# Kernel optimization log

Hardware: AMD Instinct MI355X
Metric: run time of the kernel (lower is better)

The kernel has to match this reference:

```python
import jax, jax.numpy as jnp
import numpy as np

N, MAX_DEG, F_IN, F_OUT = 20000, 32, 128, 128
TRIM_RATIO = 0.45
N_NEIGH_THRESHOLD = 3


def setup_inputs() -> dict:
    key = jax.random.key(0)
    k_h, k_nbr, k_deg, k_w, k_b = jax.random.split(key, 5)
    h = jax.random.normal(k_h, (N, F_IN), dtype=jnp.float32)
    nbr = jax.random.randint(k_nbr, (N, MAX_DEG), 0, N, dtype=jnp.int32)
    # in-degree in [1, MAX_DEG] so every node has at least one neighbor
    deg = jax.random.randint(k_deg, (N,), 1, MAX_DEG + 1, dtype=jnp.int32)
    # GCN symmetric normalizer deg^-0.5, per node, shape [N, 1]
    norm = (deg.astype(jnp.float32) ** -0.5)[:, None]
    stdv = 1.0 / np.sqrt(F_OUT)
    weight = jax.random.uniform(k_w, (F_IN, F_OUT), jnp.float32, -stdv, stdv)
    bias = jax.random.uniform(k_b, (F_OUT,), jnp.float32, -stdv, stdv)
    return {"h": h, "norm": norm, "weight": weight, "bias": bias,
            "nbr": nbr, "deg": deg}


def reference(h, norm, weight, bias, nbr, deg):
    # h: [N,F] node features (dropout=0 so input_ft == dropped_h == h)
    # nbr: [N,D] padded src indices; deg: [N] valid neighbor counts; norm: [N,1]
    D = nbr.shape[1]
    slot = jnp.arange(D, dtype=deg.dtype)[None, :]            # [1,D]
    valid = slot < deg[:, None]                                # [N,D]

    h_nbr = h[nbr]                                             # [N,D,F] = mailbox input_ft
    msg = h_nbr * norm[nbr]                                    # [N,D,F] = mailbox m (src h * src norm)

    # padded slots -> +inf so they sort past all valid entries (ranks >= deg)
    big = jnp.asarray(jnp.finfo(h.dtype).max, h.dtype)
    ift = jnp.where(valid[..., None], h_nbr, big)
    sidx = jnp.argsort(ift, axis=1)                            # per-feature sort over neighbors
    gathered = jnp.take_along_axis(msg, sidx, axis=1)          # [N,D,F]

    n = deg                                                    # per-node n_neigh
    b_raw = n // 2 - (1 - n % 2)
    b_cap = jnp.floor(n.astype(jnp.float32) * TRIM_RATIO).astype(n.dtype)
    b = jnp.maximum(jnp.minimum(b_raw, b_cap), 1)              # trim count per node

    # keep sorted ranks in [b, n-b)
    sel = (slot >= b[:, None]) & (slot < (n - b)[:, None])     # [N,D]
    trimmed_sum = jnp.sum(gathered * sel[..., None].astype(h.dtype), axis=1)  # [N,F]

    self0 = h * norm                                           # dst h * dst norm (mailbox 'self'[:,0])
    alpha = (2 * b).astype(h.dtype)[:, None]
    accum_med = (trimmed_sum + self0 * alpha) * norm           # trim_compensate=True branch
    accum_small = (n.astype(h.dtype)[:, None] * self0) * norm  # n_neigh <= threshold branch
    accum = jnp.where((n <= N_NEIGH_THRESHOLD)[:, None], accum_small, accum_med)

    # NodeApplyModule_V2: linear + bias + relu
    out = jax.nn.relu(accum @ weight + bias)
    return out
```

## Files before the change

### kernel.cpp

```cpp
#include <hip/hip_runtime.h>
#include <cfloat>
#include <cmath>

#define N_NODES 20000
#define MAXD 32
#define F 128


template <int SZ, int NV>
__device__ __forceinline__ void oe_sort_n(float (&a)[SZ]) {
#pragma unroll
  for (int p = 1; p < SZ; p <<= 1) {
#pragma unroll
    for (int q = p; q >= 1; q >>= 1) {
#pragma unroll
      for (int j = q % p; j <= SZ - 1 - q; j += 2 * q) {
#pragma unroll
        for (int i = 0; i < q; ++i) {
          int x = i + j, y = i + j + q;
          if (y < NV && (x / (2 * p)) == (y / (2 * p))) {
            float mn = fminf(a[x], a[y]);
            float mx = fmaxf(a[x], a[y]);
            a[x] = mn;
            a[y] = mx;
          }
        }
      }
    }
  }
}

template <int N>
struct TrimB {
  static constexpr int b_raw = N / 2 - (1 - (N & 1));
  static constexpr int b_cap = (int)((float)N * 0.45f);
  static constexpr int b_min = b_raw < b_cap ? b_raw : b_cap;
  static constexpr int value = b_min > 1 ? b_min : 1;
};

template <int SZ, int N>
__device__ __forceinline__ float trimmed_sum_n(const float* __restrict__ h,
                                               const float* __restrict__ norm,
                                               const int* __restrict__ nbr_row,
                                               int f) {
  constexpr int B = TrimB<N>::value;
  constexpr int NB = N - B;

  float ko[SZ];
  float nrm[SZ];
  float k[SZ];
#pragma unroll
  for (int d = 0; d < N; ++d) {
    int src = nbr_row[d];
    nrm[d] = norm[src];
    ko[d] = h[src * F + f];
    k[d] = ko[d];
  }
#pragma unroll
  for (int d = N; d < SZ; ++d) k[d] = FLT_MAX;

  oe_sort_n<SZ, N>(k);

  const float lo  = k[B];
  const float hi  = k[NB - 1];
  const float lom = k[B - 1];
  const float him = k[NB];

  float sum = 0.f;
  if ((lom < lo) & (hi < him)) {
#pragma unroll
    for (int d = 0; d < N; ++d) {
      bool keep = (ko[d] >= lo) & (ko[d] <= hi);
      sum = fmaf(keep ? ko[d] : 0.f, nrm[d], sum);
    }
  } else {
    int c_lt_lo = 0, c_lt_hi = 0;
#pragma unroll
    for (int d = 0; d < N; ++d) {
      c_lt_lo += (ko[d] < lo) ? 1 : 0;
      c_lt_hi += (ko[d] < hi) ? 1 : 0;
    }
    int run_lo = 0, run_hi = 0;
#pragma unroll
    for (int d = 0; d < N; ++d) {
      const float kd = ko[d];
      const float m = kd * nrm[d];
      const bool eql = (kd == lo);
      const bool eqh = (kd == hi);
      const bool lh = (lo < hi);
      const bool btw = (kd > lo) & (kd < hi);
      const int r_lo = c_lt_lo + run_lo;
      const int r_hi = c_lt_hi + run_hi;
      const bool inc = btw
                     | (eql & (r_lo >= B) & (lh | (r_lo < NB)))
                     | (lh & eqh & (r_hi < NB));
      sum += inc ? m : 0.f;
      run_lo += eql ? 1 : 0;
      run_hi += eqh ? 1 : 0;
    }
  }
  return sum;
}

__global__ __launch_bounds__(128) void gcn_stage1(const float* __restrict__ h,
                                                  const float* __restrict__ norm,
                                                  const int* __restrict__ nbr,
                                                  const int* __restrict__ deg,
                                                  float* __restrict__ accum) {
  const int i = blockIdx.x;
  const int f = threadIdx.x;
  const int n = deg[i];
  const float ni = norm[i];
  const float hif = h[i * F + f];
  const int idx = i * F + f;

  if (n <= 3) {
    accum[idx] = (float)n * hif * ni * ni;
    return;
  }

  const int* nbr_row = nbr + i * MAXD;
  float ts;
  int b;
  switch (n) {
#define TS_CASE(NN, SS) \
    case NN: ts = trimmed_sum_n<SS, NN>(h, norm, nbr_row, f); b = TrimB<NN>::value; break;
    TS_CASE(4, 4)
    TS_CASE(5, 8) TS_CASE(6, 8) TS_CASE(7, 8) TS_CASE(8, 8)
    TS_CASE(9, 16) TS_CASE(10, 16) TS_CASE(11, 16) TS_CASE(12, 16)
    TS_CASE(13, 16) TS_CASE(14, 16) TS_CASE(15, 16) TS_CASE(16, 16)
    TS_CASE(17, 32) TS_CASE(18, 32) TS_CASE(19, 32) TS_CASE(20, 32)
    TS_CASE(21, 32) TS_CASE(22, 32) TS_CASE(23, 32) TS_CASE(24, 32)
    TS_CASE(25, 32) TS_CASE(26, 32) TS_CASE(27, 32) TS_CASE(28, 32)
    TS_CASE(29, 32) TS_CASE(30, 32) TS_CASE(31, 32)
    default: ts = trimmed_sum_n<32, 32>(h, norm, nbr_row, f); b = TrimB<32>::value; break;
#undef TS_CASE
  }

  accum[idx] = (ts + hif * ni * (float)(2 * b)) * ni;
}

__global__ __launch_bounds__(256) void gcn_gemm(const float* __restrict__ A,
                                                const float* __restrict__ W,
                                                const float* __restrict__ bias,
                                                float* __restrict__ out) {
  __shared__ float Ws[32 * F];
  __shared__ float As[32 * 36];
  const int t = threadIdx.x;
  const int tx = t & 31;
  const int ty = t >> 5;
  const int row0 = blockIdx.x * 32;
  const int ar = t >> 3, ak = t & 7;

  float acc[4][4];
#pragma unroll
  for (int r = 0; r < 4; ++r)
#pragma unroll
    for (int c = 0; c < 4; ++c) acc[r][c] = 0.f;

#pragma unroll 1
  for (int kc = 0; kc < F; kc += 32) {
    __syncthreads();
    float4 av = *(const float4*)(A + (row0 + ar) * F + kc + ak * 4);
    *(float4*)(As + ar * 36 + ak * 4) = av;
#pragma unroll
    for (int u = 0; u < 4; ++u) {
      int idx2 = u * 256 + t;
      *(float4*)(Ws + idx2 * 4) = *(const float4*)(W + kc * F + idx2 * 4);
    }
    __syncthreads();
#pragma unroll
    for (int kq = 0; kq < 8; ++kq) {
      float4 w0 = *(const float4*)(Ws + (kq * 4 + 0) * F + tx * 4);
      float4 w1 = *(const float4*)(Ws + (kq * 4 + 1) * F + tx * 4);
      float4 w2 = *(const float4*)(Ws + (kq * 4 + 2) * F + tx * 4);
      float4 w3 = *(const float4*)(Ws + (kq * 4 + 3) * F + tx * 4);
#pragma unroll
      for (int r = 0; r < 4; ++r) {
        float4 a = *(const float4*)(As + (ty * 4 + r) * 36 + kq * 4);
        acc[r][0] = fmaf(a.x, w0.x, acc[r][0]);
        acc[r][1] = fmaf(a.x, w0.y, acc[r][1]);
        acc[r][2] = fmaf(a.x, w0.z, acc[r][2]);
        acc[r][3] = fmaf(a.x, w0.w, acc[r][3]);
        acc[r][0] = fmaf(a.y, w1.x, acc[r][0]);
        acc[r][1] = fmaf(a.y, w1.y, acc[r][1]);
        acc[r][2] = fmaf(a.y, w1.z, acc[r][2]);
        acc[r][3] = fmaf(a.y, w1.w, acc[r][3]);
        acc[r][0] = fmaf(a.z, w2.x, acc[r][0]);
        acc[r][1] = fmaf(a.z, w2.y, acc[r][1]);
        acc[r][2] = fmaf(a.z, w2.z, acc[r][2]);
        acc[r][3] = fmaf(a.z, w2.w, acc[r][3]);
        acc[r][0] = fmaf(a.w, w3.x, acc[r][0]);
        acc[r][1] = fmaf(a.w, w3.y, acc[r][1]);
        acc[r][2] = fmaf(a.w, w3.z, acc[r][2]);
        acc[r][3] = fmaf(a.w, w3.w, acc[r][3]);
      }
    }
  }

  float4 bv = *(const float4*)(bias + tx * 4);
#pragma unroll
  for (int r = 0; r < 4; ++r) {
    float4 o;
    o.x = fmaxf(acc[r][0] + bv.x, 0.f);
    o.y = fmaxf(acc[r][1] + bv.y, 0.f);
    o.z = fmaxf(acc[r][2] + bv.z, 0.f);
    o.w = fmaxf(acc[r][3] + bv.w, 0.f);
    *(float4*)(out + (row0 + ty * 4 + r) * F + tx * 4) = o;
  }
}

extern "C" void kernel_launch(void* const* d_in, const int* in_sizes, int n_in,
                              void* d_out, int out_size, void* d_ws, size_t ws_size,
                              hipStream_t stream) {
  const float* h = (const float*)d_in[0];
  const float* norm = (const float*)d_in[1];
  const float* weight = (const float*)d_in[2];
  const float* bias = (const float*)d_in[3];
  const int* nbr = (const int*)d_in[4];
  const int* deg = (const int*)d_in[5];
  float* out = (float*)d_out;
  float* accum = (float*)d_ws;

  gcn_stage1<<<N_NODES, 128, 0, stream>>>(h, norm, nbr, deg, accum);
  gcn_gemm<<<N_NODES / 32, 256, 0, stream>>>(accum, weight, bias, out);
}
```

Before: 112.1 us.

## Run GEMM on MFMA using split fp16 hi/lo operands

The first stage now writes its accumulator as two fp16 arrays, a high part and a low residual. The scalar FP32 shared-memory GEMM is replaced by a 16x16x32 fp16 MFMA GEMM that recovers near-FP32 accuracy with three products per tile (hi*hi, hi*lo, lo*hi). Each block converts the full weight matrix into transposed hi/lo fp16 tiles in LDS. This trades extra MFMA work and per-block weight conversion for matrix-core throughput. It also risks small accuracy loss and reads padded rows past N in the last block, which are never written.

Result: slower. 116.4 us (+3.9%).

```diff
diff --git a/kernel.cpp b/kernel.cpp
--- a/kernel.cpp
+++ b/kernel.cpp
@@ -1,10 +1,19 @@
 #include <hip/hip_runtime.h>
+#include <hip/hip_fp16.h>
 #include <cfloat>
 #include <cmath>
 
 #define N_NODES 20000
 #define MAXD 32
 #define F 128
+
+#define MTILE 64
+#define NBLK ((N_NODES + MTILE - 1) / MTILE)
+#define MPAD (NBLK * MTILE)
+#define WT_PITCH 136
+
+typedef _Float16 half8 __attribute__((ext_vector_type(8)));
+typedef float f32x4 __attribute__((ext_vector_type(4)));
 
 
 template <int SZ, int NV>
@@ -102,11 +111,20 @@
   return sum;
 }
 
+__device__ __forceinline__ void store_split(_Float16* __restrict__ Ah,
+                                            _Float16* __restrict__ Al,
+                                            int idx, float v) {
+  _Float16 hi = (_Float16)v;
+  Ah[idx] = hi;
+  Al[idx] = (_Float16)(v - (float)hi);
+}
+
 __global__ __launch_bounds__(128) void gcn_stage1(const float* __restrict__ h,
                                                   const float* __restrict__ norm,
                                                   const int* __restrict__ nbr,
                                                   const int* __restrict__ deg,
-                                                  float* __restrict__ accum) {
+                                                  _Float16* __restrict__ Ah,
+                                                  _Float16* __restrict__ Al) {
   const int i = blockIdx.x;
   const int f = threadIdx.x;
   const int n = deg[i];
@@ -115,7 +133,7 @@
   const int idx = i * F + f;
 
   if (n <= 3) {
-    accum[idx] = (float)n * hif * ni * ni;
+    store_split(Ah, Al, idx, (float)n * hif * ni * ni);
     return;
   }
 
@@ -137,76 +155,80 @@
 #undef TS_CASE
   }
 
-  accum[idx] = (ts + hif * ni * (float)(2 * b)) * ni;
-}
-
-__global__ __launch_bounds__(256) void gcn_gemm(const float* __restrict__ A,
-                                                const float* __restrict__ W,
-                                                const float* __restrict__ bias,
-                                                float* __restrict__ out) {
-  __shared__ float Ws[32 * F];
-  __shared__ float As[32 * 36];
+  store_split(Ah, Al, idx, (ts + hif * ni * (float)(2 * b)) * ni);
+}
+
+__global__ __launch_bounds__(256) void gcn_gemm_mfma(
+    const _Float16* __restrict__ Ah, const _Float16* __restrict__ Al,
+    const float* __restrict__ W, const float* __restrict__ bias,
+    float* __restrict__ out) {
+  __shared__ _Float16 Wt[2][F][WT_PITCH];
   const int t = threadIdx.x;
-  const int tx = t & 31;
-  const int ty = t >> 5;
-  const int row0 = blockIdx.x * 32;
-  const int ar = t >> 3, ak = t & 7;
-
-  float acc[4][4];
-#pragma unroll
-  for (int r = 0; r < 4; ++r)
-#pragma unroll
-    for (int c = 0; c < 4; ++c) acc[r][c] = 0.f;
-
-#pragma unroll 1
+
+#pragma unroll 4
+  for (int i = 0; i < 64; ++i) {
+    int idx = i * 256 + t;
+    int k = idx >> 7, n = idx & 127;
+    float w = W[idx];
+    _Float16 hi = (_Float16)w;
+    Wt[0][n][k] = hi;
+    Wt[1][n][k] = (_Float16)(w - (float)hi);
+  }
+  __syncthreads();
+
+  const int lane = t & 63;
+  const int wv = t >> 6;
+  const int l16 = lane & 15;
+  const int kg = lane >> 4;
+  const int row0 = blockIdx.x * MTILE;
+  const int colb = wv * 32;
+
+  f32x4 acc[4][2];
+#pragma unroll
+  for (int rf = 0; rf < 4; ++rf)
+#pragma unroll
+    for (int cf = 0; cf < 2; ++cf) acc[rf][cf] = (f32x4){0.f, 0.f, 0.f, 0.f};
+
+#pragma unroll
   for (int kc = 0; kc < F; kc += 32) {
-    __syncthreads();
-    float4 av = *(const float4*)(A + (row0 + ar) * F + kc + ak * 4);
-    *(float4*)(As + ar * 36 + ak * 4) = av;
-#pragma unroll
-    for (int u = 0; u < 4; ++u) {
-      int idx2 = u * 256 + t;
-      *(float4*)(Ws + idx2 * 4) = *(const float4*)(W + kc * F + idx2 * 4);
-    }
-    __syncthreads();
-#pragma unroll
-    for (int kq = 0; kq < 8; ++kq) {
-      float4 w0 = *(const float4*)(Ws + (kq * 4 + 0) * F + tx * 4);
-      float4 w1 = *(const float4*)(Ws + (kq * 4 + 1) * F + tx * 4);
-      float4 w2 = *(const float4*)(Ws + (kq * 4 + 2) * F + tx * 4);
-      float4 w3 = *(const float4*)(Ws + (kq * 4 + 3) * F + tx * 4);
+    half8 ah[4], al[4], bh[2], bl[2];
+#pragma unroll
+    for (int rf = 0; rf < 4; ++rf) {
+      const int row = row0 + rf * 16 + l16;
+      const size_t off = (size_t)row * F + kc + kg * 8;
+      ah[rf] = *(const half8*)(Ah + off);
+      al[rf] = *(const half8*)(Al + off);
+    }
+#pragma unroll
+    for (int cf = 0; cf < 2; ++cf) {
+      const int n = colb + cf * 16 + l16;
+      bh[cf] = *(const half8*)(&Wt[0][n][kc + kg * 8]);
+      bl[cf] = *(const half8*)(&Wt[1][n][kc + kg * 8]);
+    }
+#pragma unroll
+    for (int rf = 0; rf < 4; ++rf)
+#pragma unroll
+      for (int cf = 0; cf < 2; ++cf) {
+        acc[rf][cf] = __builtin_amdgcn_mfma_f32_16x16x32_f16(ah[rf], bh[cf], acc[rf][cf], 0, 0, 0);
+        acc[rf][cf] = __builtin_amdgcn_mfma_f32_16x16x32_f16(ah[rf], bl[cf], acc[rf][cf], 0, 0, 0);
+        acc[rf][cf] = __builtin_amdgcn_mfma_f32_16x16x32_f16(al[rf], bh[cf], acc[rf][cf], 0, 0, 0);
+      }
+  }
+
+#pragma unroll
+  for (int cf = 0; cf < 2; ++cf) {
+    const int col = colb + cf * 16 + l16;
+    const float bv = bias[col];
+#pragma unroll
+    for (int rf = 0; rf < 4; ++rf) {
 #pragma unroll
       for (int r = 0; r < 4; ++r) {
-        float4 a = *(const float4*)(As + (ty * 4 + r) * 36 + kq * 4);
-        acc[r][0] = fmaf(a.x, w0.x, acc[r][0]);
-        acc[r][1] = fmaf(a.x, w0.y, acc[r][1]);
-        acc[r][2] = fmaf(a.x, w0.z, acc[r][2]);
-        acc[r][3] = fmaf(a.x, w0.w, acc[r][3]);
-        acc[r][0] = fmaf(a.y, w1.x, acc[r][0]);
-        acc[r][1] = fmaf(a.y, w1.y, acc[r][1]);
-        acc[r][2] = fmaf(a.y, w1.z, acc[r][2]);
-        acc[r][3] = fmaf(a.y, w1.w, acc[r][3]);
-        acc[r][0] = fmaf(a.z, w2.x, acc[r][0]);
-        acc[r][1] = fmaf(a.z, w2.y, acc[r][1]);
-        acc[r][2] = fmaf(a.z, w2.z, acc[r][2]);
-        acc[r][3] = fmaf(a.z, w2.w, acc[r][3]);
-        acc[r][0] = fmaf(a.w, w3.x, acc[r][0]);
-        acc[r][1] = fmaf(a.w, w3.y, acc[r][1]);
-        acc[r][2] = fmaf(a.w, w3.z, acc[r][2]);
-        acc[r][3] = fmaf(a.w, w3.w, acc[r][3]);
+        const int row = row0 + rf * 16 + kg * 4 + r;
+        if (row < N_NODES) {
+          out[(size_t)row * F + col] = fmaxf(acc[rf][cf][r] + bv, 0.f);
+        }
       }
     }
-  }
-
-  float4 bv = *(const float4*)(bias + tx * 4);
-#pragma unroll
-  for (int r = 0; r < 4; ++r) {
-    float4 o;
-    o.x = fmaxf(acc[r][0] + bv.x, 0.f);
-    o.y = fmaxf(acc[r][1] + bv.y, 0.f);
-    o.z = fmaxf(acc[r][2] + bv.z, 0.f);
-    o.w = fmaxf(acc[r][3] + bv.w, 0.f);
-    *(float4*)(out + (row0 + ty * 4 + r) * F + tx * 4) = o;
   }
 }
 
@@ -220,8 +242,10 @@
   const int* nbr = (const int*)d_in[4];
   const int* deg = (const int*)d_in[5];
   float* out = (float*)d_out;
-  float* accum = (float*)d_ws;
-
-  gcn_stage1<<<N_NODES, 128, 0, stream>>>(h, norm, nbr, deg, accum);
-  gcn_gemm<<<N_NODES / 32, 256, 0, stream>>>(accum, weight, bias, out);
-}
+
+  _Float16* Ah = (_Float16*)d_ws;
+  _Float16* Al = Ah + (size_t)MPAD * F;
+
+  gcn_stage1<<<N_NODES, 128, 0, stream>>>(h, norm, nbr, deg, Ah, Al);
+  gcn_gemm_mfma<<<NBLK, 256, 0, stream>>>(Ah, Al, weight, bias, out);
+}
```
